# Optimization experiments

Hardware: AMD Instinct MI355X
Metric: run time of the kernel (lower is better)

The kernel has to match this reference:

```python
import jax, jax.numpy as jnp
import numpy as np

N = 100000   # nodes
E = 1000000  # edges
F_IN = 15    # node feature dim
H = 64       # hidden dim
EMB = 128    # embedding dim
R = 13       # relations
NB = 4       # bases


def _xavier(key, shape):
    fan_in, fan_out = shape[-2], shape[-1]
    lim = float(np.sqrt(6.0 / (fan_in + fan_out)))
    return jax.random.uniform(key, shape, jnp.float32, -lim, lim)


def setup_inputs() -> dict:
    key = jax.random.key(0)
    ks = jax.random.split(key, 24)
    inp = {}
    inp["node_features"] = jax.random.normal(ks[0], (N, F_IN), jnp.float32)
    inp["edge_index"] = jax.random.randint(ks[1], (2, E), 0, N, jnp.int32)
    inp["edge_type"] = jax.random.randint(ks[2], (E,), 0, R, jnp.int32)
    # input projection (15 -> 64)
    inp["W_in"] = _xavier(ks[3], (F_IN, H)); inp["b_in"] = jnp.zeros((H,), jnp.float32)
    # RGCN layer 0
    inp["Wself0"] = _xavier(ks[4], (H, H)); inp["bself0"] = jnp.zeros((H,), jnp.float32)
    inp["bases0"] = _xavier(ks[5], (NB, H, H))
    inp["coeffs0"] = _xavier(ks[6], (R, NB))
    # RGCN layer 1
    inp["Wself1"] = _xavier(ks[7], (H, H)); inp["bself1"] = jnp.zeros((H,), jnp.float32)
    inp["bases1"] = _xavier(ks[8], (NB, H, H))
    inp["coeffs1"] = _xavier(ks[9], (R, NB))
    # readout MLP (2H -> H -> EMB)
    inp["Wr1"] = _xavier(ks[10], (2 * H, H)); inp["br1"] = jnp.zeros((H,), jnp.float32)
    inp["Wr2"] = _xavier(ks[11], (H, EMB)); inp["br2"] = jnp.zeros((EMB,), jnp.float32)
    # node projection (H -> EMB)
    inp["Wnp"] = _xavier(ks[12], (H, EMB)); inp["bnp"] = jnp.zeros((EMB,), jnp.float32)
    return inp


def _rgcn_layer(h, src, tgt, etype, Wself, bself, bases, coeffs):
    # h: (N, H). Sum over relations of per-relation gather+matmul+scatter-add
    # == single scatter over all edges with per-edge relation weight.
    # Basis decomposition: W_r = sum_b coeffs[r,b] * bases[b].
    h_src = h[src]                 # (E, H) gather
    c_e = coeffs[etype]            # (E, NB) per-edge basis coefficients
    msg = jnp.zeros((h_src.shape[0], bases.shape[2]), h.dtype)
    for b in range(bases.shape[0]):  # fixed small loop over NB=4 bases
        msg = msg + c_e[:, b:b + 1] * (h_src @ bases[b])
    agg = jax.ops.segment_sum(msg, tgt, num_segments=h.shape[0])  # (N, H)
    # NOTE: original code computes degree norm but never applies it (dead code),
    # so aggregation is an unnormalized scatter-add, reproduced faithfully here.
    return jax.nn.relu(h @ Wself + bself + agg)  # dropout is identity in eval


def reference(node_features, edge_index, edge_type, W_in, b_in,
              Wself0, bself0, bases0, coeffs0,
              Wself1, bself1, bases1, coeffs1,
              Wr1, br1, Wr2, br2, Wnp, bnp):
    src, tgt = edge_index[0], edge_index[1]
    h = node_features @ W_in + b_in                      # (N, H)
    h = _rgcn_layer(h, src, tgt, edge_type, Wself0, bself0, bases0, coeffs0)
    h = _rgcn_layer(h, src, tgt, edge_type, Wself1, bself1, bases1, coeffs1)
    # graph readout: mean + max pooling over nodes -> MLP
    g = jnp.concatenate([h.mean(axis=0), h.max(axis=0)])  # (2H,)
    graph_emb = jax.nn.relu(g @ Wr1 + br1) @ Wr2 + br2    # (EMB,)
    node_emb = h @ Wnp + bnp                              # (N, EMB)
    return graph_emb, node_emb
```

## Files before the change

### kernel.cpp

```cpp
#include <hip/hip_runtime.h>
#include <hip/hip_bf16.h>

#define NN 100000
#define EE 1000000
#define FIN 15
#define HH 64
#define EMBD 128
#define RR 13
#define NBASE 4
#define NP 391
#define CAP 1700128
#define SENT (15 << 17)
#define LYB (NN / 16)

typedef __hip_bfloat16 bf16;
typedef __attribute__((ext_vector_type(8))) short short8;
typedef __attribute__((ext_vector_type(4))) float f32x4;

__device__ __forceinline__ float b2f(bf16 x) { return __bfloat162float(x); }
__device__ __forceinline__ float bcast(float v, int l) {
    return __uint_as_float(__builtin_amdgcn_readlane(__float_as_uint(v), l));
}
__device__ __forceinline__ int bcasti(int v, int l) {
    return (int)__builtin_amdgcn_readlane((unsigned)v, l);
}
__device__ __forceinline__ unsigned short f2bu(float f) {
    bf16 t = __float2bfloat16(f);
    return *reinterpret_cast<unsigned short*>(&t);
}
__device__ __forceinline__ float bu2f(unsigned u) {
    return __uint_as_float(u << 16);
}

__global__ void k_detect(const void* __restrict__ win, int* __restrict__ flag) {
    int tid = threadIdx.x;
    const bf16* p = (const bf16*)win;
    int cnt = 0;
    for (int i = tid; i < FIN * HH; i += 64) {
        float v = b2f(p[i]);
        if (!(fabsf(v) < 0.3f)) cnt++;
    }
#pragma unroll
    for (int off = 32; off > 0; off >>= 1) cnt += __shfl_down(cnt, off, 64);
    if (tid == 0) *flag = (cnt > 40) ? 1 : 0;
}

struct ConvTab {
    const void* in[17];
    int n[17];
    int cum[18];
};

__global__ void k_convert_all(ConvTab tab, float* __restrict__ base,
                              const int* __restrict__ flag) {
    int g = blockIdx.x * 256 + threadIdx.x;
    if (g >= tab.cum[17]) return;
    int t = 0;
#pragma unroll
    for (int i = 0; i < 17; ++i) if (g >= tab.cum[i + 1]) t = i + 1;
    int local = g - tab.cum[t];
    if (local >= tab.n[t]) return;
    float v;
    if (*flag) v = ((const float*)tab.in[t])[local];
    else       v = b2f(((const bf16*)tab.in[t])[local]);
    base[g] = v;
}

__global__ void k_zero(int* __restrict__ a, int n) {
    int i = blockIdx.x * 256 + threadIdx.x;
    if (i < n) a[i] = 0;
}

__global__ void k_fill(int* __restrict__ a, int n, int val) {
    int i = blockIdx.x * 256 + threadIdx.x;
    if (i < n) a[i] = val;
}

__global__ void k_hist(const int* __restrict__ tgt, int* __restrict__ count,
                       int* __restrict__ rank) {
    int e = blockIdx.x * 256 + threadIdx.x;
    if (e >= EE) return;
    rank[e] = atomicAdd(&count[tgt[e]], 1);
}

__global__ void k_scan1(const int* __restrict__ count, int* __restrict__ scanned,
                        int* __restrict__ partials) {
    __shared__ int buf[256];
    int tid = threadIdx.x;
    int i = blockIdx.x * 256 + tid;
    int v = (i < NN) ? ((count[i] + 7) & ~7) : 0;
    buf[tid] = v;
    __syncthreads();
    for (int off = 1; off < 256; off <<= 1) {
        int t = (tid >= off) ? buf[tid - off] : 0;
        __syncthreads();
        buf[tid] += t;
        __syncthreads();
    }
    if (i < NN) scanned[i] = buf[tid] - v;
    if (tid == 255) partials[blockIdx.x] = buf[255];
}

__global__ void k_scan2(int* __restrict__ partials) {
    __shared__ int buf[512];
    int tid = threadIdx.x;
    int v = (tid < NP) ? partials[tid] : 0;
    buf[tid] = v;
    __syncthreads();
    for (int off = 1; off < 512; off <<= 1) {
        int t = (tid >= off) ? buf[tid - off] : 0;
        __syncthreads();
        buf[tid] += t;
        __syncthreads();
    }
    if (tid < NP) partials[tid] = buf[tid] - v;
}

__global__ void k_scatter(const int* __restrict__ src, const int* __restrict__ tgt,
                          const int* __restrict__ et, const int* __restrict__ rank,
                          const int* __restrict__ scanned, const int* __restrict__ partials,
                          int* __restrict__ packed) {
    int e = blockIdx.x * 256 + threadIdx.x;
    if (e >= EE) return;
    int t = tgt[e];
    int pos = scanned[t] + partials[t >> 8] + rank[e];
    packed[pos] = src[e] | (et[e] << 17);
}

__global__ void k_coef(const float* __restrict__ c0, const float* __restrict__ c1,
                       float* __restrict__ o0, float* __restrict__ o1) {
    int t = threadIdx.x;
    int r = t >> 2, b = t & 3;
    o0[t] = (r < RR) ? c0[r * NBASE + b] : 0.f;
    o1[t] = (r < RR) ? c1[r * NBASE + b] : 0.f;
}

__global__ void k_wcat(const float* __restrict__ bases0, const float* __restrict__ Wself0,
                       const float* __restrict__ bases1, const float* __restrict__ Wself1,
                       unsigned short* __restrict__ W0, unsigned short* __restrict__ W1) {
    int idx = blockIdx.x * 256 + threadIdx.x;
    if (idx >= HH * 320) return;
    int n = idx / 320, k = idx - n * 320;
    int b = k >> 6, kk = k & 63;
    float v0 = (b < 4) ? bases0[b * 4096 + kk * 64 + n] : Wself0[kk * 64 + n];
    float v1 = (b < 4) ? bases1[b * 4096 + kk * 64 + n] : Wself1[kk * 64 + n];
    W0[idx] = f2bu(v0);
    W1[idx] = f2bu(v1);
}

__global__ void k_wt(const float* __restrict__ Wnp, unsigned short* __restrict__ WT) {
    int idx = blockIdx.x * 256 + threadIdx.x;
    if (idx >= EMBD * HH) return;
    int c = idx >> 6, k = idx & 63;
    float w = Wnp[k * EMBD + c];
    unsigned short hi = f2bu(w);
    WT[idx] = hi;
    WT[EMBD * HH + idx] = f2bu(w - bu2f(hi));
}


__global__ void k_input_proj(const float* __restrict__ nf, const float* __restrict__ Win,
                             const float* __restrict__ bin, unsigned short* __restrict__ h) {
    __shared__ float w[FIN * HH];
    __shared__ float bb[HH];
    int tid = threadIdx.x;
    for (int i = tid; i < FIN * HH; i += 256) w[i] = Win[i];
    if (tid < HH) bb[tid] = bin[tid];
    __syncthreads();
    int idx = blockIdx.x * 256 + tid;
    if (idx >= NN * HH) return;
    int n = idx >> 6, j = idx & 63;
    float acc = bb[j];
    const float* row = nf + n * FIN;
#pragma unroll
    for (int k = 0; k < FIN; ++k) acc = fmaf(row[k], w[k * HH + j], acc);
    h[idx] = f2bu(acc);
}

__device__ __forceinline__ void edge_group16(const unsigned short* __restrict__ hin,
                                             const float* __restrict__ cc,
                                             int lane, int pk, int j, float S[4]) {
    float hv[16];
    int rr[16];
#pragma unroll
    for (int k = 0; k < 16; ++k) {
        int v = bcasti(pk, j + k);
        rr[k] = (v >> 17) & 0xF;
        hv[k] = bu2f((unsigned)hin[(v & 0x1FFFF) * HH + lane]);
    }
#pragma unroll
    for (int hh = 0; hh < 2; ++hh) {
        float4 cv[8];
#pragma unroll
        for (int k = 0; k < 8; ++k)
            cv[k] = *(const float4*)(cc + rr[hh * 8 + k] * 4);
#pragma unroll
        for (int k = 0; k < 8; ++k) {
            float hk = hv[hh * 8 + k];
            S[0] = fmaf(cv[k].x, hk, S[0]);
            S[1] = fmaf(cv[k].y, hk, S[1]);
            S[2] = fmaf(cv[k].z, hk, S[2]);
            S[3] = fmaf(cv[k].w, hk, S[3]);
        }
    }
}

__device__ __forceinline__ void edge_group8(const unsigned short* __restrict__ hin,
                                            const float* __restrict__ cc,
                                            int lane, int pk, int j, float S[4]) {
    float hv[8];
    int rr[8];
#pragma unroll
    for (int k = 0; k < 8; ++k) {
        int v = bcasti(pk, j + k);
        rr[k] = (v >> 17) & 0xF;
        hv[k] = bu2f((unsigned)hin[(v & 0x1FFFF) * HH + lane]);
    }
    float4 cv[8];
#pragma unroll
    for (int k = 0; k < 8; ++k) cv[k] = *(const float4*)(cc + rr[k] * 4);
#pragma unroll
    for (int k = 0; k < 8; ++k) {
        float hk = hv[k];
        S[0] = fmaf(cv[k].x, hk, S[0]);
        S[1] = fmaf(cv[k].y, hk, S[1]);
        S[2] = fmaf(cv[k].z, hk, S[2]);
        S[3] = fmaf(cv[k].w, hk, S[3]);
    }
}

__device__ __forceinline__ void gather_node(const unsigned short* __restrict__ hin,
                                            const int* __restrict__ packed,
                                            const float* __restrict__ cc,
                                            int lane, int pk, int s0, int cntp,
                                            float S[4]) {
    int lim = min(64, cntp);
    int j = 0;
    for (; j + 16 <= lim; j += 16) edge_group16(hin, cc, lane, pk, j, S);
    if (j < lim) edge_group8(hin, cc, lane, pk, j, S);
    for (int base = 64; base < cntp; base += 64) {
        int pkx = packed[s0 + base + lane];
        int lim2 = min(64, cntp - base);
        int j2 = 0;
        for (; j2 + 16 <= lim2; j2 += 16) edge_group16(hin, cc, lane, pkx, j2, S);
        if (j2 < lim2) edge_group8(hin, cc, lane, pkx, j2, S);
    }
}

template <int TAIL>
__global__ void __launch_bounds__(256, 6)
k_layer(const unsigned short* __restrict__ hin, const int* __restrict__ packed,
        const int* __restrict__ count, const int* __restrict__ scanned,
        const int* __restrict__ partials, const float* __restrict__ cc,
        const unsigned short* __restrict__ Wc, const float* __restrict__ bself,
        unsigned short* __restrict__ hout,
        const unsigned short* __restrict__ WT, const float* __restrict__ bnp,
        void* __restrict__ out, const int* __restrict__ flag,
        float* __restrict__ psum, float* __restrict__ pmax) {
    __shared__ __align__(16) unsigned short Sb[16 * 264];
    int tid = threadIdx.x;
    int lane = tid & 63;
    int wv = tid >> 6;
    int t0 = blockIdx.x * 16;
    int nb = t0 + wv * 4;

    int4 c4  = *(const int4*)(count + nb);
    int4 sc4 = *(const int4*)(scanned + nb);
    int pb = partials[t0 >> 8];
    int s00 = sc4.x + pb, s01 = sc4.y + pb, s02 = sc4.z + pb, s03 = sc4.w + pb;
    int cp0 = (c4.x + 7) & ~7, cp1 = (c4.y + 7) & ~7;
    int cp2 = (c4.z + 7) & ~7, cp3 = (c4.w + 7) & ~7;

    int pk0 = packed[s00 + lane];
    int pk1 = packed[s01 + lane];
    int pk2 = packed[s02 + lane];
    int pk3 = packed[s03 + lane];

    float S0[4] = {0, 0, 0, 0}, S1[4] = {0, 0, 0, 0};
    float S2[4] = {0, 0, 0, 0}, S3[4] = {0, 0, 0, 0};
    gather_node(hin, packed, cc, lane, pk0, s00, cp0, S0);
    gather_node(hin, packed, cc, lane, pk1, s01, cp1, S1);
    gather_node(hin, packed, cc, lane, pk2, s02, cp2, S2);
    gather_node(hin, packed, cc, lane, pk3, s03, cp3, S3);

#pragma unroll
    for (int b = 0; b < NBASE; ++b) {
        Sb[(wv * 4 + 0) * 264 + b * 64 + lane] = f2bu(S0[b]);
        Sb[(wv * 4 + 1) * 264 + b * 64 + lane] = f2bu(S1[b]);
        Sb[(wv * 4 + 2) * 264 + b * 64 + lane] = f2bu(S2[b]);
        Sb[(wv * 4 + 3) * 264 + b * 64 + lane] = f2bu(S3[b]);
    }
    __syncthreads();

    int m16 = lane & 15;
    int g = lane >> 4;
    f32x4 acc = {0.f, 0.f, 0.f, 0.f};
    const unsigned short* brow = Wc + (wv * 16 + m16) * 320 + g * 8;
#pragma unroll
    for (int kb = 0; kb < 8; ++kb) {
        short8 a = *(const short8*)(&Sb[m16 * 264 + kb * 32 + g * 8]);
        short8 b = *(const short8*)(brow + kb * 32);
        acc = __builtin_amdgcn_mfma_f32_16x16x32_bf16(a, b, acc, 0, 0, 0);
    }
    const unsigned short* hrow = hin + (t0 + m16) * HH + g * 8;
#pragma unroll
    for (int kb = 0; kb < 2; ++kb) {
        short8 a = *(const short8*)(hrow + kb * 32);
        short8 b = *(const short8*)(brow + 256 + kb * 32);
        acc = __builtin_amdgcn_mfma_f32_16x16x32_bf16(a, b, acc, 0, 0, 0);
    }
    int col = wv * 16 + m16;
    float bias = bself[col];

    if (TAIL == 0) {
#pragma unroll
        for (int r = 0; r < 4; ++r) {
            int row = g * 4 + r;
            hout[(t0 + row) * HH + col] = f2bu(fmaxf(acc[r] + bias, 0.f));
        }
        return;
    }

    __syncthreads();
#pragma unroll
    for (int r = 0; r < 4; ++r)
        Sb[(g * 4 + r) * 264 + col] = f2bu(fmaxf(acc[r] + bias, 0.f));
    __syncthreads();

    const unsigned short* ar = &Sb[m16 * 264 + g * 8];
    short8 a0 = *(const short8*)(ar);
    short8 a1 = *(const short8*)(ar + 32);
    int c0 = wv * 32;
    const unsigned short* bp0 = WT + (c0 + m16) * HH + g * 8;
    const unsigned short* bp1 = WT + (c0 + 16 + m16) * HH + g * 8;
    const unsigned short* lp0 = bp0 + EMBD * HH;
    const unsigned short* lp1 = bp1 + EMBD * HH;

    f32x4 eA = {0.f, 0.f, 0.f, 0.f}, eB = {0.f, 0.f, 0.f, 0.f};
    eA = __builtin_amdgcn_mfma_f32_16x16x32_bf16(a0, *(const short8*)bp0, eA, 0, 0, 0);
    eA = __builtin_amdgcn_mfma_f32_16x16x32_bf16(a1, *(const short8*)(bp0 + 32), eA, 0, 0, 0);
    eA = __builtin_amdgcn_mfma_f32_16x16x32_bf16(a0, *(const short8*)lp0, eA, 0, 0, 0);
    eA = __builtin_amdgcn_mfma_f32_16x16x32_bf16(a1, *(const short8*)(lp0 + 32), eA, 0, 0, 0);
    eB = __builtin_amdgcn_mfma_f32_16x16x32_bf16(a0, *(const short8*)bp1, eB, 0, 0, 0);
    eB = __builtin_amdgcn_mfma_f32_16x16x32_bf16(a1, *(const short8*)(bp1 + 32), eB, 0, 0, 0);
    eB = __builtin_amdgcn_mfma_f32_16x16x32_bf16(a0, *(const short8*)lp1, eB, 0, 0, 0);
    eB = __builtin_amdgcn_mfma_f32_16x16x32_bf16(a1, *(const short8*)(lp1 + 32), eB, 0, 0, 0);

    float biasA = bnp[c0 + m16], biasB = bnp[c0 + 16 + m16];
    if (*flag) {
        float* o = (float*)out + EMBD;
#pragma unroll
        for (int r = 0; r < 4; ++r) {
            long node = t0 + g * 4 + r;
            o[node * EMBD + c0 + m16]      = eA[r] + biasA;
            o[node * EMBD + c0 + 16 + m16] = eB[r] + biasB;
        }
    } else {
        bf16* o = (bf16*)out + EMBD;
#pragma unroll
        for (int r = 0; r < 4; ++r) {
            long node = t0 + g * 4 + r;
            o[node * EMBD + c0 + m16]      = __float2bfloat16(eA[r] + biasA);
            o[node * EMBD + c0 + 16 + m16] = __float2bfloat16(eB[r] + biasB);
        }
    }

    if (wv == 0) {
        float s = 0.f, m = -1e30f;
#pragma unroll
        for (int r16 = 0; r16 < 16; ++r16) {
            float v = bu2f((unsigned)Sb[r16 * 264 + lane]);
            s += v;
            m = fmaxf(m, v);
        }
        psum[blockIdx.x * 64 + lane] = s;
        pmax[blockIdx.x * 64 + lane] = m;
    }
}

__global__ void k_reduce2(const float* __restrict__ psum, const float* __restrict__ pmax,
                          float* __restrict__ psum2, float* __restrict__ pmax2) {
    __shared__ float ls[256], lm[256];
    int tid = threadIdx.x;
    int j = tid & 63;
    int slot = tid >> 6;
    float s = 0.f, m = -1e30f;
    for (int n = blockIdx.x * 4 + slot; n < LYB; n += 256 * 4) {
        s += psum[n * 64 + j];
        m = fmaxf(m, pmax[n * 64 + j]);
    }
    ls[tid] = s; lm[tid] = m;
    __syncthreads();
    if (tid < 64) {
        s = ls[tid] + ls[tid + 64] + ls[tid + 128] + ls[tid + 192];
        m = fmaxf(fmaxf(lm[tid], lm[tid + 64]), fmaxf(lm[tid + 128], lm[tid + 192]));
        psum2[blockIdx.x * 64 + tid] = s;
        pmax2[blockIdx.x * 64 + tid] = m;
    }
}

__global__ void k_finish(const float* __restrict__ psum, const float* __restrict__ pmax,
                         const float* __restrict__ Wr1, const float* __restrict__ br1,
                         const float* __restrict__ Wr2, const float* __restrict__ br2,
                         void* __restrict__ out, const int* __restrict__ flag) {
    __shared__ float ls[256], lm[256];
    __shared__ float g[2 * HH];
    __shared__ float tbuf[HH];
    int tid = threadIdx.x;
    int j = tid & 63;
    int slot = tid >> 6;
    float s = 0.f, m = -1e30f;
    for (int i = slot; i < 256; i += 4) {
        s += psum[i * 64 + j];
        m = fmaxf(m, pmax[i * 64 + j]);
    }
    ls[tid] = s; lm[tid] = m;
    __syncthreads();
    if (tid < 64) {
        s = ls[tid] + ls[tid + 64] + ls[tid + 128] + ls[tid + 192];
        m = fmaxf(fmaxf(lm[tid], lm[tid + 64]), fmaxf(lm[tid + 128], lm[tid + 192]));
        g[tid] = s * (1.0f / NN);
        g[64 + tid] = m;
    }
    __syncthreads();
    if (tid < 64) {
        float acc = br1[tid];
#pragma unroll 8
        for (int k = 0; k < 2 * HH; ++k) acc = fmaf(g[k], Wr1[k * HH + tid], acc);
        tbuf[tid] = fmaxf(acc, 0.f);
    }
    __syncthreads();
    if (tid < EMBD) {
        float acc = br2[tid];
#pragma unroll 8
        for (int k = 0; k < HH; ++k) acc = fmaf(tbuf[k], Wr2[k * EMBD + tid], acc);
        if (*flag) ((float*)out)[tid] = acc;
        else       ((bf16*)out)[tid] = __float2bfloat16(acc);
    }
}

extern "C" void kernel_launch(void* const* d_in, const int* in_sizes, int n_in,
                              void* d_out, int out_size, void* d_ws, size_t ws_size,
                              hipStream_t stream) {
    const int* eidx  = (const int*)d_in[1];
    const int* etype = (const int*)d_in[2];
    const int* src = eidx;
    const int* tgt = eidx + EE;

    int* flag = (int*)d_ws;
    float* base = (float*)d_ws + 16;

    const int fidx[17] = {0, 3, 4, 5, 6, 7, 8, 9, 10, 11, 12, 13, 14, 15, 16, 17, 18};
    ConvTab tab;
    float* conv[19];
    int cum = 0;
    for (int t = 0; t < 17; ++t) {
        int i = fidx[t];
        tab.in[t] = d_in[i];
        tab.n[t] = in_sizes[i];
        tab.cum[t] = cum;
        conv[i] = base + cum;
        cum += (in_sizes[i] + 15) & ~15;
    }
    tab.cum[17] = cum;

    k_detect<<<1, 64, 0, stream>>>(d_in[3], flag);
    k_convert_all<<<(cum + 255) / 256, 256, 0, stream>>>(tab, base, flag);

    float* p = base + cum;
    float* psum  = p;  p += LYB * 64;
    float* pmax  = p;  p += LYB * 64;
    float* psum2 = p;  p += 256 * 64;
    float* pmax2 = p;  p += 256 * 64;
    float* c16a = p;  p += 64;
    float* c16b = p;  p += 64;
    int* count    = (int*)p;           p += NN;
    int* scanned  = (int*)p;           p += NN;
    int* partials = (int*)p;           p += 512;
    int* rank     = (int*)p;           p += EE;
    int* packed   = (int*)p;           p += CAP;
    unsigned short* hbf0 = (unsigned short*)p;
    unsigned short* hbf1 = hbf0 + (size_t)NN * HH;
    unsigned short* Wc0  = hbf1 + (size_t)NN * HH;
    unsigned short* Wc1  = Wc0 + HH * 320;
    unsigned short* WT   = Wc1 + HH * 320;

    const float* nf      = conv[0];
    const float* Win     = conv[3];
    const float* bin     = conv[4];
    const float* Wself0  = conv[5];
    const float* bself0  = conv[6];
    const float* bases0  = conv[7];
    const float* coeffs0 = conv[8];
    const float* Wself1  = conv[9];
    const float* bself1  = conv[10];
    const float* bases1  = conv[11];
    const float* coeffs1 = conv[12];
    const float* Wr1     = conv[13];
    const float* br1     = conv[14];
    const float* Wr2     = conv[15];
    const float* br2     = conv[16];
    const float* Wnp     = conv[17];
    const float* bnp     = conv[18];

    const int NHB = (NN * HH) / 256;
    const int EB  = (EE + 255) / 256;

    k_zero<<<(NN + 255) / 256, 256, 0, stream>>>(count, NN);
    k_fill<<<(CAP + 255) / 256, 256, 0, stream>>>(packed, CAP, SENT);
    k_hist<<<EB, 256, 0, stream>>>(tgt, count, rank);
    k_scan1<<<NP, 256, 0, stream>>>(count, scanned, partials);
    k_scan2<<<1, 512, 0, stream>>>(partials);
    k_scatter<<<EB, 256, 0, stream>>>(src, tgt, etype, rank, scanned, partials, packed);

    k_coef<<<1, 64, 0, stream>>>(coeffs0, coeffs1, c16a, c16b);
    k_wcat<<<(HH * 320 + 255) / 256, 256, 0, stream>>>(bases0, Wself0, bases1, Wself1, Wc0, Wc1);
    k_wt<<<(EMBD * HH + 255) / 256, 256, 0, stream>>>(Wnp, WT);
    k_input_proj<<<NHB, 256, 0, stream>>>(nf, Win, bin, hbf0);

    k_layer<0><<<LYB, 256, 0, stream>>>(hbf0, packed, count, scanned, partials, c16a, Wc0, bself0,
                                        hbf1, nullptr, nullptr, nullptr, nullptr, nullptr, nullptr);
    k_layer<1><<<LYB, 256, 0, stream>>>(hbf1, packed, count, scanned, partials, c16b, Wc1, bself1,
                                        hbf0, WT, bnp, d_out, flag, psum, pmax);

    k_reduce2<<<256, 256, 0, stream>>>(psum, pmax, psum2, pmax2);
    k_finish<<<1, 256, 0, stream>>>(psum2, pmax2, Wr1, br1, Wr2, br2, d_out, flag);
}
```

Measured before the change: 392.8 us.

## Merge small setup kernels into fused launches with last-block ticket reductions

Cuts the launch count by folding detect, convert, zero, fill and coefficient prep into one kernel with block-range dispatch. Scatter, weight repacking and input projection go into a second combined kernel. The two-pass scan and the reduce/finish pairs now use an atomic ticket so the last block finishes the work inside the same launch. This removes several kernel launches and their serialization gaps, at the cost of every convert block recomputing the dtype-detect reduction and extra fences for the tickets.

```diff
diff --git a/kernel.cpp b/kernel.cpp
--- a/kernel.cpp
+++ b/kernel.cpp
@@ -13,14 +13,18 @@
 #define SENT (15 << 17)
 #define LYB (NN / 16)
 
+#define ZB 391
+#define FB 6642
+#define SC_B 3907
+#define WC_B 80
+#define WT_B 32
+#define IP_B 25000
+
 typedef __hip_bfloat16 bf16;
 typedef __attribute__((ext_vector_type(8))) short short8;
 typedef __attribute__((ext_vector_type(4))) float f32x4;
 
 __device__ __forceinline__ float b2f(bf16 x) { return __bfloat162float(x); }
-__device__ __forceinline__ float bcast(float v, int l) {
-    return __uint_as_float(__builtin_amdgcn_readlane(__float_as_uint(v), l));
-}
 __device__ __forceinline__ int bcasti(int v, int l) {
     return (int)__builtin_amdgcn_readlane((unsigned)v, l);
 }
@@ -32,17 +36,22 @@
     return __uint_as_float(u << 16);
 }
 
-__global__ void k_detect(const void* __restrict__ win, int* __restrict__ flag) {
+__device__ __forceinline__ int detect_flag(const void* __restrict__ win) {
+    __shared__ int cs[256];
     int tid = threadIdx.x;
     const bf16* p = (const bf16*)win;
     int cnt = 0;
-    for (int i = tid; i < FIN * HH; i += 64) {
+    for (int i = tid; i < FIN * HH; i += 256) {
         float v = b2f(p[i]);
         if (!(fabsf(v) < 0.3f)) cnt++;
     }
-#pragma unroll
-    for (int off = 32; off > 0; off >>= 1) cnt += __shfl_down(cnt, off, 64);
-    if (tid == 0) *flag = (cnt > 40) ? 1 : 0;
+    cs[tid] = cnt;
+    __syncthreads();
+    for (int off = 128; off > 0; off >>= 1) {
+        if (tid < off) cs[tid] += cs[tid + off];
+        __syncthreads();
+    }
+    return (cs[0] > 40) ? 1 : 0;
 }
 
 struct ConvTab {
@@ -51,29 +60,52 @@
     int cum[18];
 };
 
-__global__ void k_convert_all(ConvTab tab, float* __restrict__ base,
-                              const int* __restrict__ flag) {
-    int g = blockIdx.x * 256 + threadIdx.x;
-    if (g >= tab.cum[17]) return;
-    int t = 0;
-#pragma unroll
-    for (int i = 0; i < 17; ++i) if (g >= tab.cum[i + 1]) t = i + 1;
-    int local = g - tab.cum[t];
-    if (local >= tab.n[t]) return;
-    float v;
-    if (*flag) v = ((const float*)tab.in[t])[local];
-    else       v = b2f(((const bf16*)tab.in[t])[local]);
-    base[g] = v;
-}
-
-__global__ void k_zero(int* __restrict__ a, int n) {
-    int i = blockIdx.x * 256 + threadIdx.x;
-    if (i < n) a[i] = 0;
-}
-
-__global__ void k_fill(int* __restrict__ a, int n, int val) {
-    int i = blockIdx.x * 256 + threadIdx.x;
-    if (i < n) a[i] = val;
+__global__ void k_convert_init(ConvTab tab, float* __restrict__ base,
+                               int* __restrict__ flagp,
+                               int* __restrict__ count, int* __restrict__ packed,
+                               const void* __restrict__ c0raw, const void* __restrict__ c1raw,
+                               float* __restrict__ o0, float* __restrict__ o1,
+                               const void* __restrict__ win, int CB) {
+    int b = blockIdx.x;
+    int tid = threadIdx.x;
+    if (b < CB) {
+        int flag = detect_flag(win);
+        if (b == 0 && tid < 3) flagp[tid] = (tid == 0) ? flag : 0;
+        int g = b * 256 + tid;
+        if (g >= tab.cum[17]) return;
+        int t = 0;
+#pragma unroll
+        for (int i = 0; i < 17; ++i) if (g >= tab.cum[i + 1]) t = i + 1;
+        int local = g - tab.cum[t];
+        if (local >= tab.n[t]) return;
+        base[g] = flag ? ((const float*)tab.in[t])[local]
+                       : b2f(((const bf16*)tab.in[t])[local]);
+        return;
+    }
+    b -= CB;
+    if (b < ZB) {
+        int i = b * 256 + tid;
+        if (i < NN) count[i] = 0;
+        return;
+    }
+    b -= ZB;
+    if (b < FB) {
+        int i = b * 256 + tid;
+        if (i < CAP) packed[i] = SENT;
+        return;
+    }
+    int flag = detect_flag(win);
+    if (tid < 64) {
+        int r = tid >> 2, bb = tid & 3;
+        float v0 = 0.f, v1 = 0.f;
+        if (r < RR) {
+            int i = r * NBASE + bb;
+            v0 = flag ? ((const float*)c0raw)[i] : b2f(((const bf16*)c0raw)[i]);
+            v1 = flag ? ((const float*)c1raw)[i] : b2f(((const bf16*)c1raw)[i]);
+        }
+        o0[tid] = v0;
+        o1[tid] = v1;
+    }
 }
 
 __global__ void k_hist(const int* __restrict__ tgt, int* __restrict__ count,
@@ -83,9 +115,10 @@
     rank[e] = atomicAdd(&count[tgt[e]], 1);
 }
 
-__global__ void k_scan1(const int* __restrict__ count, int* __restrict__ scanned,
-                        int* __restrict__ partials) {
+__global__ void k_scan1f(const int* __restrict__ count, int* __restrict__ scanned,
+                         int* __restrict__ partials, int* __restrict__ ticket) {
     __shared__ int buf[256];
+    __shared__ int lastFlag;
     int tid = threadIdx.x;
     int i = blockIdx.x * 256 + tid;
     int v = (i < NN) ? ((count[i] + 7) & ~7) : 0;
@@ -99,82 +132,94 @@
     }
     if (i < NN) scanned[i] = buf[tid] - v;
     if (tid == 255) partials[blockIdx.x] = buf[255];
-}
-
-__global__ void k_scan2(int* __restrict__ partials) {
-    __shared__ int buf[512];
+
+    __syncthreads();
+    if (tid == 0) {
+        __threadfence();
+        lastFlag = (__hip_atomic_fetch_add(ticket, 1, __ATOMIC_ACQ_REL,
+                                           __HIP_MEMORY_SCOPE_AGENT) == NP - 1);
+        __threadfence();
+    }
+    __syncthreads();
+    if (!lastFlag) return;
+
+    __shared__ int b2[512];
+    int v0 = (tid < NP) ? partials[tid] : 0;
+    int v1 = (tid + 256 < NP) ? partials[tid + 256] : 0;
+    b2[tid] = v0;
+    b2[tid + 256] = v1;
+    __syncthreads();
+    for (int off = 1; off < 512; off <<= 1) {
+        int t0 = (tid >= off) ? b2[tid - off] : 0;
+        int t1 = (tid + 256 >= off) ? b2[tid + 256 - off] : 0;
+        __syncthreads();
+        b2[tid] += t0;
+        b2[tid + 256] += t1;
+        __syncthreads();
+    }
+    if (tid < NP) partials[tid] = b2[tid] - v0;
+    if (tid + 256 < NP) partials[tid + 256] = b2[tid + 256] - v1;
+}
+
+__global__ void k_mid(const int* __restrict__ src, const int* __restrict__ tgt,
+                      const int* __restrict__ et, const int* __restrict__ rank,
+                      const int* __restrict__ scanned, const int* __restrict__ partials,
+                      int* __restrict__ packed,
+                      const float* __restrict__ bases0, const float* __restrict__ Wself0,
+                      const float* __restrict__ bases1, const float* __restrict__ Wself1,
+                      unsigned short* __restrict__ W0, unsigned short* __restrict__ W1,
+                      const float* __restrict__ Wnp, unsigned short* __restrict__ WT,
+                      const float* __restrict__ nf, const float* __restrict__ Win,
+                      const float* __restrict__ bin, unsigned short* __restrict__ h) {
+    int b = blockIdx.x;
     int tid = threadIdx.x;
-    int v = (tid < NP) ? partials[tid] : 0;
-    buf[tid] = v;
-    __syncthreads();
-    for (int off = 1; off < 512; off <<= 1) {
-        int t = (tid >= off) ? buf[tid - off] : 0;
+    if (b < SC_B) {
+        int e = b * 256 + tid;
+        if (e >= EE) return;
+        int t = tgt[e];
+        int pos = scanned[t] + partials[t >> 8] + rank[e];
+        packed[pos] = src[e] | (et[e] << 17);
+        return;
+    }
+    b -= SC_B;
+    if (b < WC_B) {
+        int idx = b * 256 + tid;
+        if (idx >= HH * 320) return;
+        int n = idx / 320, k = idx - n * 320;
+        int bb = k >> 6, kk = k & 63;
+        float v0 = (bb < 4) ? bases0[bb * 4096 + kk * 64 + n] : Wself0[kk * 64 + n];
+        float v1 = (bb < 4) ? bases1[bb * 4096 + kk * 64 + n] : Wself1[kk * 64 + n];
+        W0[idx] = f2bu(v0);
+        W1[idx] = f2bu(v1);
+        return;
+    }
+    b -= WC_B;
+    if (b < WT_B) {
+        int idx = b * 256 + tid;
+        if (idx >= EMBD * HH) return;
+        int c = idx >> 6, k = idx & 63;
+        float w = Wnp[k * EMBD + c];
+        unsigned short hi = f2bu(w);
+        WT[idx] = hi;
+        WT[EMBD * HH + idx] = f2bu(w - bu2f(hi));
+        return;
+    }
+    b -= WT_B;
+    {
+        __shared__ float w[FIN * HH];
+        __shared__ float bb[HH];
+        for (int i = tid; i < FIN * HH; i += 256) w[i] = Win[i];
+        if (tid < HH) bb[tid] = bin[tid];
         __syncthreads();
-        buf[tid] += t;
-        __syncthreads();
-    }
-    if (tid < NP) partials[tid] = buf[tid] - v;
-}
-
-__global__ void k_scatter(const int* __restrict__ src, const int* __restrict__ tgt,
-                          const int* __restrict__ et, const int* __restrict__ rank,
-                          const int* __restrict__ scanned, const int* __restrict__ partials,
-                          int* __restrict__ packed) {
-    int e = blockIdx.x * 256 + threadIdx.x;
-    if (e >= EE) return;
-    int t = tgt[e];
-    int pos = scanned[t] + partials[t >> 8] + rank[e];
-    packed[pos] = src[e] | (et[e] << 17);
-}
-
-__global__ void k_coef(const float* __restrict__ c0, const float* __restrict__ c1,
-                       float* __restrict__ o0, float* __restrict__ o1) {
-    int t = threadIdx.x;
-    int r = t >> 2, b = t & 3;
-    o0[t] = (r < RR) ? c0[r * NBASE + b] : 0.f;
-    o1[t] = (r < RR) ? c1[r * NBASE + b] : 0.f;
-}
-
-__global__ void k_wcat(const float* __restrict__ bases0, const float* __restrict__ Wself0,
-                       const float* __restrict__ bases1, const float* __restrict__ Wself1,
-                       unsigned short* __restrict__ W0, unsigned short* __restrict__ W1) {
-    int idx = blockIdx.x * 256 + threadIdx.x;
-    if (idx >= HH * 320) return;
-    int n = idx / 320, k = idx - n * 320;
-    int b = k >> 6, kk = k & 63;
-    float v0 = (b < 4) ? bases0[b * 4096 + kk * 64 + n] : Wself0[kk * 64 + n];
-    float v1 = (b < 4) ? bases1[b * 4096 + kk * 64 + n] : Wself1[kk * 64 + n];
-    W0[idx] = f2bu(v0);
-    W1[idx] = f2bu(v1);
-}
-
-__global__ void k_wt(const float* __restrict__ Wnp, unsigned short* __restrict__ WT) {
-    int idx = blockIdx.x * 256 + threadIdx.x;
-    if (idx >= EMBD * HH) return;
-    int c = idx >> 6, k = idx & 63;
-    float w = Wnp[k * EMBD + c];
-    unsigned short hi = f2bu(w);
-    WT[idx] = hi;
-    WT[EMBD * HH + idx] = f2bu(w - bu2f(hi));
-}
-
-
-__global__ void k_input_proj(const float* __restrict__ nf, const float* __restrict__ Win,
-                             const float* __restrict__ bin, unsigned short* __restrict__ h) {
-    __shared__ float w[FIN * HH];
-    __shared__ float bb[HH];
-    int tid = threadIdx.x;
-    for (int i = tid; i < FIN * HH; i += 256) w[i] = Win[i];
-    if (tid < HH) bb[tid] = bin[tid];
-    __syncthreads();
-    int idx = blockIdx.x * 256 + tid;
-    if (idx >= NN * HH) return;
-    int n = idx >> 6, j = idx & 63;
-    float acc = bb[j];
-    const float* row = nf + n * FIN;
-#pragma unroll
-    for (int k = 0; k < FIN; ++k) acc = fmaf(row[k], w[k * HH + j], acc);
-    h[idx] = f2bu(acc);
+        int idx = b * 256 + tid;
+        if (idx >= NN * HH) return;
+        int n = idx >> 6, j = idx & 63;
+        float acc = bb[j];
+        const float* row = nf + n * FIN;
+#pragma unroll
+        for (int k = 0; k < FIN; ++k) acc = fmaf(row[k], w[k * HH + j], acc);
+        h[idx] = f2bu(acc);
+    }
 }
 
 __device__ __forceinline__ void edge_group16(const unsigned short* __restrict__ hin,
@@ -378,9 +423,16 @@
     }
 }
 
-__global__ void k_reduce2(const float* __restrict__ psum, const float* __restrict__ pmax,
-                          float* __restrict__ psum2, float* __restrict__ pmax2) {
+__global__ void k_reduce2f(const float* __restrict__ psum, const float* __restrict__ pmax,
+                           float* __restrict__ psum2, float* __restrict__ pmax2,
+                           const float* __restrict__ Wr1, const float* __restrict__ br1,
+                           const float* __restrict__ Wr2, const float* __restrict__ br2,
+                           void* __restrict__ out, const int* __restrict__ flag,
+                           int* __restrict__ ticket) {
     __shared__ float ls[256], lm[256];
+    __shared__ float g[2 * HH];
+    __shared__ float tbuf[HH];
+    __shared__ int lastFlag;
     int tid = threadIdx.x;
     int j = tid & 63;
     int slot = tid >> 6;
@@ -397,22 +449,21 @@
         psum2[blockIdx.x * 64 + tid] = s;
         pmax2[blockIdx.x * 64 + tid] = m;
     }
-}
-
-__global__ void k_finish(const float* __restrict__ psum, const float* __restrict__ pmax,
-                         const float* __restrict__ Wr1, const float* __restrict__ br1,
-                         const float* __restrict__ Wr2, const float* __restrict__ br2,
-                         void* __restrict__ out, const int* __restrict__ flag) {
-    __shared__ float ls[256], lm[256];
-    __shared__ float g[2 * HH];
-    __shared__ float tbuf[HH];
-    int tid = threadIdx.x;
-    int j = tid & 63;
-    int slot = tid >> 6;
-    float s = 0.f, m = -1e30f;
+    __syncthreads();
+
+    if (tid == 0) {
+        __threadfence();
+        lastFlag = (__hip_atomic_fetch_add(ticket, 1, __ATOMIC_ACQ_REL,
+                                           __HIP_MEMORY_SCOPE_AGENT) == 255);
+        __threadfence();
+    }
+    __syncthreads();
+    if (!lastFlag) return;
+
+    s = 0.f; m = -1e30f;
     for (int i = slot; i < 256; i += 4) {
-        s += psum[i * 64 + j];
-        m = fmaxf(m, pmax[i * 64 + j]);
+        s += psum2[i * 64 + j];
+        m = fmaxf(m, pmax2[i * 64 + j]);
     }
     ls[tid] = s; lm[tid] = m;
     __syncthreads();
@@ -463,9 +514,6 @@
         cum += (in_sizes[i] + 15) & ~15;
     }
     tab.cum[17] = cum;
-
-    k_detect<<<1, 64, 0, stream>>>(d_in[3], flag);
-    k_convert_all<<<(cum + 255) / 256, 256, 0, stream>>>(tab, base, flag);
 
     float* p = base + cum;
     float* psum  = p;  p += LYB * 64;
@@ -491,11 +539,9 @@
     const float* Wself0  = conv[5];
     const float* bself0  = conv[6];
     const float* bases0  = conv[7];
-    const float* coeffs0 = conv[8];
     const float* Wself1  = conv[9];
     const float* bself1  = conv[10];
     const float* bases1  = conv[11];
-    const float* coeffs1 = conv[12];
     const float* Wr1     = conv[13];
     const float* br1     = conv[14];
     const float* Wr2     = conv[15];
@@ -503,26 +549,20 @@
     const float* Wnp     = conv[17];
     const float* bnp     = conv[18];
 
-    const int NHB = (NN * HH) / 256;
-    const int EB  = (EE + 255) / 256;
-
-    k_zero<<<(NN + 255) / 256, 256, 0, stream>>>(count, NN);
-    k_fill<<<(CAP + 255) / 256, 256, 0, stream>>>(packed, CAP, SENT);
+    const int CB = (cum + 255) / 256;
+    const int EB = (EE + 255) / 256;
+
+    k_convert_init<<<CB + ZB + FB + 1, 256, 0, stream>>>(
+        tab, base, flag, count, packed, d_in[8], d_in[12], c16a, c16b, d_in[3], CB);
     k_hist<<<EB, 256, 0, stream>>>(tgt, count, rank);
-    k_scan1<<<NP, 256, 0, stream>>>(count, scanned, partials);
-    k_scan2<<<1, 512, 0, stream>>>(partials);
-    k_scatter<<<EB, 256, 0, stream>>>(src, tgt, etype, rank, scanned, partials, packed);
-
-    k_coef<<<1, 64, 0, stream>>>(coeffs0, coeffs1, c16a, c16b);
-    k_wcat<<<(HH * 320 + 255) / 256, 256, 0, stream>>>(bases0, Wself0, bases1, Wself1, Wc0, Wc1);
-    k_wt<<<(EMBD * HH + 255) / 256, 256, 0, stream>>>(Wnp, WT);
-    k_input_proj<<<NHB, 256, 0, stream>>>(nf, Win, bin, hbf0);
-
+    k_scan1f<<<NP, 256, 0, stream>>>(count, scanned, partials, flag + 1);
+    k_mid<<<SC_B + WC_B + WT_B + IP_B, 256, 0, stream>>>(
+        src, tgt, etype, rank, scanned, partials, packed,
+        bases0, Wself0, bases1, Wself1, Wc0, Wc1, Wnp, WT, nf, Win, bin, hbf0);
     k_layer<0><<<LYB, 256, 0, stream>>>(hbf0, packed, count, scanned, partials, c16a, Wc0, bself0,
                                         hbf1, nullptr, nullptr, nullptr, nullptr, nullptr, nullptr);
     k_layer<1><<<LYB, 256, 0, stream>>>(hbf1, packed, count, scanned, partials, c16b, Wc1, bself1,
                                         hbf0, WT, bnp, d_out, flag, psum, pmax);
-
-    k_reduce2<<<256, 256, 0, stream>>>(psum, pmax, psum2, pmax2);
-    k_finish<<<1, 256, 0, stream>>>(psum2, pmax2, Wr1, br1, Wr2, br2, d_out, flag);
-}
+    k_reduce2f<<<256, 256, 0, stream>>>(psum, pmax, psum2, pmax2,
+                                        Wr1, br1, Wr2, br2, d_out, flag, flag + 2);
+}
```

Result: no change. 397.0 us (+1.1%).
